# Kernel optimization log

Hardware: AMD Instinct MI355X
Metric: run time of the kernel (lower is better)

Reference implementation:

```python
import jax, jax.numpy as jnp
import numpy as np

N_RELS = 8           # NUM_BASE_RELS(6) + 2
CONF_LOG_WEIGHT = 0.1
LN_EPS = 1e-5


def setup_inputs() -> dict:
    key = jax.random.key(0)
    ks = jax.random.split(key, 10)
    N, E, IN, H, R, L = 100000, 1600000, 128, 64, 16, 2
    x = jax.random.normal(ks[0], (N, IN), jnp.float32)
    edge_index = jax.random.randint(ks[1], (2, E), 0, N, jnp.int32)
    edge_type = jax.random.randint(ks[2], (E,), 0, N_RELS, jnp.int32)
    edge_attr = jax.random.uniform(ks[3], (E, 1), jnp.float32)

    def init(k, shape, fan_in):
        return jax.random.normal(k, shape, jnp.float32) * (1.0 / np.sqrt(fan_in))

    W_in = init(ks[4], (IN, H), IN)
    b_in = jnp.zeros((H,), jnp.float32)
    W_msg = init(ks[5], (L, H, H), H)          # msg_lin, no bias
    rel_emb = init(ks[6], (L, N_RELS, R), 1.0)  # relation embedding tables
    W_relproj = init(ks[7], (L, R, H), R)       # rel_proj, no bias
    att_vec = init(ks[8], (L, 3 * H), 3 * H)
    bias = jnp.zeros((L, H), jnp.float32)
    ln_g = jnp.ones((L, H), jnp.float32)
    ln_b = jnp.zeros((L, H), jnp.float32)
    return dict(x=x, W_in=W_in, b_in=b_in, W_msg=W_msg, rel_emb=rel_emb,
                W_relproj=W_relproj, att_vec=att_vec, bias=bias,
                ln_g=ln_g, ln_b=ln_b, edge_attr=edge_attr,
                edge_index=edge_index, edge_type=edge_type)


def _layer(h, src, dst, t, conf, W_msg, rel_emb, W_relproj, att_vec, bias, N, H):
    h_src = h[src] @ W_msg                      # [E,H] gather + linear
    h_dst = h[dst] @ W_msg                      # [E,H]
    r = rel_emb[t] @ W_relproj                  # [E,H]
    a_dst, a_src, a_rel = att_vec[:H], att_vec[H:2 * H], att_vec[2 * H:]
    # equivalent to sum over concat([h_dst, h_src, r]) * att_vec
    e = h_dst @ a_dst + h_src @ a_src + r @ a_rel      # [E]
    e = jax.nn.leaky_relu(e, 0.2)
    e = e + CONF_LOG_WEIGHT * jnp.log(jnp.maximum(conf, 1e-6))
    # segment softmax over destination nodes
    m = jax.ops.segment_max(e, dst, num_segments=N)
    ex = jnp.exp(e - m[dst])
    s = jax.ops.segment_sum(ex, dst, num_segments=N)
    alpha = ex / s[dst]
    out = jax.ops.segment_sum(h_src * alpha[:, None], dst, num_segments=N)
    return out + bias


def _layernorm(x, g, b):
    mu = x.mean(-1, keepdims=True)
    var = ((x - mu) ** 2).mean(-1, keepdims=True)
    return (x - mu) / jnp.sqrt(var + LN_EPS) * g + b


def reference(x, W_in, b_in, W_msg, rel_emb, W_relproj, att_vec, bias, ln_g, ln_b,
              edge_attr, edge_index, edge_type):
    N, H = x.shape[0], W_in.shape[1]
    src, dst = edge_index[0], edge_index[1]
    t = jnp.clip(edge_type, 0, N_RELS - 1)
    conf = edge_attr[:, 0]
    h = jax.nn.relu(x @ W_in + b_in)            # in_lin + relu (dropout eval = id)
    for l in range(W_msg.shape[0]):
        out = _layer(h, src, dst, t, conf, W_msg[l], rel_emb[l], W_relproj[l],
                     att_vec[l], bias[l], N, H)
        h = _layernorm(h + jax.nn.relu(out), ln_g[l], ln_b[l])
    return h
```

## Files before the change

kernel.cpp:

```cpp
#include <hip/hip_runtime.h>
#include <math.h>

#define H 64
#define IN_DIM 128
#define NRELS 8
#define SCAN_B 512
#define DEGCAP 128
#define CHUNK 8192
#define MAXBUCK 512
#define BUCKSZ 2048

__global__ __launch_bounds__(256) void k_input(const float* __restrict__ x,
    const float* __restrict__ W_in, const float* __restrict__ b_in,
    float* __restrict__ h, int N) {
  __shared__ __align__(16) float Ws[IN_DIM * H];
  __shared__ __align__(16) float xs[16 * IN_DIM];
  const float4* W4 = (const float4*)W_in;
  float4* Ws4 = (float4*)Ws;
  for (int i = threadIdx.x; i < IN_DIM * H / 4; i += 256) Ws4[i] = W4[i];
  int base = blockIdx.x * 16;
  const float4* x4 = (const float4*)x;
  float4* xs4 = (float4*)xs;
  for (int i = threadIdx.x; i < 16 * IN_DIM / 4; i += 256) {
    int nn = base + (i >> 5);
    xs4[i] = (nn < N) ? x4[(size_t)nn * 32 + (i & 31)]
                      : make_float4(0.f, 0.f, 0.f, 0.f);
  }
  __syncthreads();
  int wid = threadIdx.x >> 6, lane = threadIdx.x & 63;
  int n0 = base + wid * 4;
  float a0 = 0.f, a1 = 0.f, a2 = 0.f, a3 = 0.f;
  const float4* xr4 = (const float4*)(xs + wid * 4 * IN_DIM);
  #pragma unroll 4
  for (int kq = 0; kq < IN_DIM / 4; ++kq) {
    float4 f0 = xr4[kq];
    float4 f1 = xr4[32 + kq];
    float4 f2 = xr4[64 + kq];
    float4 f3 = xr4[96 + kq];
    int k = kq * 4;
    float w0 = Ws[(k + 0) * H + lane];
    float w1 = Ws[(k + 1) * H + lane];
    float w2 = Ws[(k + 2) * H + lane];
    float w3 = Ws[(k + 3) * H + lane];
    a0 = fmaf(f0.x, w0, a0); a0 = fmaf(f0.y, w1, a0);
    a0 = fmaf(f0.z, w2, a0); a0 = fmaf(f0.w, w3, a0);
    a1 = fmaf(f1.x, w0, a1); a1 = fmaf(f1.y, w1, a1);
    a1 = fmaf(f1.z, w2, a1); a1 = fmaf(f1.w, w3, a1);
    a2 = fmaf(f2.x, w0, a2); a2 = fmaf(f2.y, w1, a2);
    a2 = fmaf(f2.z, w2, a2); a2 = fmaf(f2.w, w3, a2);
    a3 = fmaf(f3.x, w0, a3); a3 = fmaf(f3.y, w1, a3);
    a3 = fmaf(f3.z, w2, a3); a3 = fmaf(f3.w, w3, a3);
  }
  float bb = b_in[lane];
  if (n0 + 0 < N) h[(size_t)(n0 + 0) * H + lane] = fmaxf(a0 + bb, 0.f);
  if (n0 + 1 < N) h[(size_t)(n0 + 1) * H + lane] = fmaxf(a1 + bb, 0.f);
  if (n0 + 2 < N) h[(size_t)(n0 + 2) * H + lane] = fmaxf(a2 + bb, 0.f);
  if (n0 + 3 < N) h[(size_t)(n0 + 3) * H + lane] = fmaxf(a3 + bb, 0.f);
}

__global__ __launch_bounds__(SCAN_B) void k_scan1(const int* __restrict__ deg,
    int* __restrict__ inc, int* __restrict__ bsum, int N) {
  __shared__ int sm[SCAN_B];
  int g = blockIdx.x * SCAN_B + threadIdx.x;
  sm[threadIdx.x] = (g < N) ? deg[g] : 0;
  __syncthreads();
  for (int o = 1; o < SCAN_B; o <<= 1) {
    int t = (threadIdx.x >= o) ? sm[threadIdx.x - o] : 0;
    __syncthreads();
    sm[threadIdx.x] += t;
    __syncthreads();
  }
  if (g < N) inc[g] = sm[threadIdx.x];
  if (threadIdx.x == SCAN_B - 1) bsum[blockIdx.x] = sm[threadIdx.x];
}

__global__ __launch_bounds__(SCAN_B) void k_scan2(int* __restrict__ bsum, int nb) {
  __shared__ int sm[SCAN_B];
  __shared__ int carry;
  if (threadIdx.x == 0) carry = 0;
  __syncthreads();
  for (int base = 0; base < nb; base += SCAN_B) {
    int i = base + threadIdx.x;
    sm[threadIdx.x] = (i < nb) ? bsum[i] : 0;
    __syncthreads();
    if (threadIdx.x == 0) {
      int run = carry;
      int lim = nb - base < SCAN_B ? nb - base : SCAN_B;
      for (int j = 0; j < lim; ++j) { run += sm[j]; sm[j] = run; }
      carry = run;
    }
    __syncthreads();
    if (i < nb) bsum[i] = sm[threadIdx.x];
    __syncthreads();
  }
}

__global__ __launch_bounds__(SCAN_B) void k_scan3(const int* __restrict__ inc,
    const int* __restrict__ bsum, const int* __restrict__ deg,
    int* __restrict__ row, int N) {
  int g = blockIdx.x * SCAN_B + threadIdx.x;
  if (g >= N) return;
  int off = (blockIdx.x > 0) ? bsum[blockIdx.x - 1] : 0;
  int end = inc[g] + off;
  row[g] = end - deg[g];
  if (g == N - 1) row[N] = end;
}

__global__ __launch_bounds__(SCAN_B) void k_scan3b(const int* __restrict__ inc,
    const int* __restrict__ bsum, const int* __restrict__ cnt,
    int* __restrict__ woff, int M) {
  int g = blockIdx.x * SCAN_B + threadIdx.x;
  if (g >= M) return;
  int off = (blockIdx.x > 0) ? bsum[blockIdx.x - 1] : 0;
  woff[g] = inc[g] + off - cnt[g];
}

__global__ __launch_bounds__(256) void k_bhist(const int* __restrict__ ei,
    int* __restrict__ counts, int E, int nwg, int nbuck, int bshift) {
  __shared__ int cnt[MAXBUCK];
  for (int b = threadIdx.x; b < nbuck; b += 256) cnt[b] = 0;
  __syncthreads();
  int wg = blockIdx.x;
  int lo = wg * CHUNK, hi = lo + CHUNK < E ? lo + CHUNK : E;
  for (int j = lo + threadIdx.x; j < hi; j += 256)
    atomicAdd(&cnt[ei[E + j] >> bshift], 1);
  __syncthreads();
  for (int b = threadIdx.x; b < nbuck; b += 256)
    counts[(size_t)b * nwg + wg] = cnt[b];
}

__global__ __launch_bounds__(256) void k_binscat(const int* __restrict__ ei,
    const int* __restrict__ et, const float* __restrict__ ea,
    const int* __restrict__ woff, int4* __restrict__ staged,
    int E, int nwg, int nbuck, int bshift) {
  __shared__ int cur[MAXBUCK];
  int wg = blockIdx.x;
  for (int b = threadIdx.x; b < nbuck; b += 256)
    cur[b] = woff[(size_t)b * nwg + wg];
  __syncthreads();
  int lo = wg * CHUNK, hi = lo + CHUNK < E ? lo + CHUNK : E;
  for (int j = lo + threadIdx.x; j < hi; j += 256) {
    int s = ei[j], d = ei[E + j];
    int t = et[j]; t = t < 0 ? 0 : (t > NRELS - 1 ? NRELS - 1 : t);
    float cl = 0.1f * logf(fmaxf(ea[j], 1e-6f));
    int pos = atomicAdd(&cur[d >> bshift], 1);
    staged[pos] = make_int4(s | (t << 20), d, __float_as_int(cl), 0);
  }
}

__global__ __launch_bounds__(256) void k_hist2(const int* __restrict__ staged,
    const int* __restrict__ woff, int* __restrict__ deg,
    int E, int nwg, int nbuck, int bshift, int N) {
  __shared__ int cnt[BUCKSZ];
  int b = blockIdx.x;
  int nbase = b << bshift;
  int nn = N - nbase; if (nn > (1 << bshift)) nn = 1 << bshift;
  for (int i = threadIdx.x; i < nn; i += 256) cnt[i] = 0;
  __syncthreads();
  int lo = woff[(size_t)b * nwg];
  int hi = (b + 1 < nbuck) ? woff[(size_t)(b + 1) * nwg] : E;
  for (int j = lo + threadIdx.x; j < hi; j += 256)
    atomicAdd(&cnt[staged[j * 4 + 1] - nbase], 1);
  __syncthreads();
  for (int i = threadIdx.x; i < nn; i += 256) deg[nbase + i] = cnt[i];
}

__global__ __launch_bounds__(256) void k_scat2(const int4* __restrict__ staged,
    const int* __restrict__ woff, const int* __restrict__ row,
    int2* __restrict__ erec, int E, int nwg, int nbuck, int bshift, int N) {
  __shared__ int cur[BUCKSZ];
  int b = blockIdx.x;
  int nbase = b << bshift;
  int nn = N - nbase; if (nn > (1 << bshift)) nn = 1 << bshift;
  for (int i = threadIdx.x; i < nn; i += 256) cur[i] = row[nbase + i];
  __syncthreads();
  int lo = woff[(size_t)b * nwg];
  int hi = (b + 1 < nbuck) ? woff[(size_t)(b + 1) * nwg] : E;
  for (int j = lo + threadIdx.x; j < hi; j += 256) {
    int4 r = staged[j];
    int pos = atomicAdd(&cur[r.y - nbase], 1);
    erec[pos] = make_int2(r.x, r.z);
  }
}

__global__ __launch_bounds__(256) void k_node(const float* __restrict__ h,
    const float* __restrict__ Wmsg, const float* __restrict__ att,
    float* __restrict__ hw, float* __restrict__ esrc, float* __restrict__ edst,
    int N) {
  __shared__ __align__(16) float Ws[H * H];
  __shared__ __align__(16) float hs[16 * H];
  const float4* W4 = (const float4*)Wmsg;
  float4* Ws4 = (float4*)Ws;
  for (int i = threadIdx.x; i < H * H / 4; i += 256) Ws4[i] = W4[i];
  int base = blockIdx.x * 16;
  const float4* h4 = (const float4*)h;
  float4* hs4 = (float4*)hs;
  for (int i = threadIdx.x; i < 16 * H / 4; i += 256) {
    int nn = base + (i >> 4);
    hs4[i] = (nn < N) ? h4[(size_t)nn * 16 + (i & 15)]
                      : make_float4(0.f, 0.f, 0.f, 0.f);
  }
  __syncthreads();
  int wid = threadIdx.x >> 6, lane = threadIdx.x & 63;
  int n0 = base + wid * 4;
  float a0 = 0.f, a1 = 0.f, a2 = 0.f, a3 = 0.f;
  const float4* hr4 = (const float4*)(hs + wid * 4 * H);
  #pragma unroll 4
  for (int kq = 0; kq < H / 4; ++kq) {
    float4 f0 = hr4[kq];
    float4 f1 = hr4[16 + kq];
    float4 f2 = hr4[32 + kq];
    float4 f3 = hr4[48 + kq];
    int k = kq * 4;
    float w0 = Ws[(k + 0) * H + lane];
    float w1 = Ws[(k + 1) * H + lane];
    float w2 = Ws[(k + 2) * H + lane];
    float w3 = Ws[(k + 3) * H + lane];
    a0 = fmaf(f0.x, w0, a0); a0 = fmaf(f0.y, w1, a0);
    a0 = fmaf(f0.z, w2, a0); a0 = fmaf(f0.w, w3, a0);
    a1 = fmaf(f1.x, w0, a1); a1 = fmaf(f1.y, w1, a1);
    a1 = fmaf(f1.z, w2, a1); a1 = fmaf(f1.w, w3, a1);
    a2 = fmaf(f2.x, w0, a2); a2 = fmaf(f2.y, w1, a2);
    a2 = fmaf(f2.z, w2, a2); a2 = fmaf(f2.w, w3, a2);
    a3 = fmaf(f3.x, w0, a3); a3 = fmaf(f3.y, w1, a3);
    a3 = fmaf(f3.z, w2, a3); a3 = fmaf(f3.w, w3, a3);
  }
  float ad = att[lane], as = att[H + lane];
  float acc[4] = {a0, a1, a2, a3};
  #pragma unroll
  for (int i = 0; i < 4; ++i) {
    int n = n0 + i;
    if (n >= N) break;
    hw[(size_t)n * H + lane] = acc[i];
    float vd = acc[i] * ad, vs = acc[i] * as;
    #pragma unroll
    for (int o = 32; o >= 1; o >>= 1) {
      vd += __shfl_xor(vd, o);
      vs += __shfl_xor(vs, o);
    }
    if (lane == 0) { edst[n] = vd; esrc[n] = vs; }
  }
}

__global__ void k_rel(const float* __restrict__ rel_emb,
    const float* __restrict__ Wrp, const float* __restrict__ att,
    float* __restrict__ erel, int R) {
  int l = blockIdx.x;
  int r = threadIdx.x >> 6, lane = threadIdx.x & 63;
  const float* re = rel_emb + ((size_t)l * NRELS + r) * R;
  const float* wp = Wrp + (size_t)l * R * H;
  float acc = 0.f;
  for (int k = 0; k < R; ++k) acc = fmaf(re[k], wp[k * H + lane], acc);
  float v = acc * att[(size_t)l * 3 * H + 2 * H + lane];
  #pragma unroll
  for (int o = 32; o >= 1; o >>= 1) v += __shfl_xor(v, o);
  if (lane == 0) erel[l * NRELS + r] = v;
}

__global__ __launch_bounds__(256) void k_agg(const int* __restrict__ row,
    const int2* __restrict__ erec, const float* __restrict__ esrc,
    const float* __restrict__ edst, const float* __restrict__ erel,
    const float* __restrict__ hw, const float* __restrict__ h,
    const float* __restrict__ bias, const float* __restrict__ ln_g,
    const float* __restrict__ ln_b, float* __restrict__ hout, int N) {
  __shared__ float er[NRELS];
  __shared__ float els[4][DEGCAP];
  __shared__ int   sls[4][DEGCAP];
  if (threadIdx.x < NRELS) er[threadIdx.x] = erel[threadIdx.x];
  __syncthreads();
  int wid = threadIdx.x >> 6, lane = threadIdx.x & 63;
  int w = blockIdx.x * 4 + wid;
  if (w >= N) return;
  int st = row[w], en = row[w + 1];
  int deg = en - st;
  float ed = edst[w];
  float m = -3.4e38f;
  float acc = 0.f, ssum = 0.f;

  if (deg <= DEGCAP) {
    for (int j = st + lane; j < en; j += 64) {
      int2 r = erec[j];
      int sj = r.x & 0xFFFFF;
      float e = ed + esrc[sj] + er[(r.x >> 20) & 7];
      e = e > 0.f ? e : 0.2f * e;
      e += __int_as_float(r.y);
      els[wid][j - st] = e;
      sls[wid][j - st] = sj;
      m = fmaxf(m, e);
    }
    #pragma unroll
    for (int o = 32; o >= 1; o >>= 1) m = fmaxf(m, __shfl_xor(m, o));
    int k = 0;
    for (; k + 8 <= deg; k += 8) {
      int s0 = sls[wid][k],     s1 = sls[wid][k + 1];
      int s2 = sls[wid][k + 2], s3 = sls[wid][k + 3];
      int s4 = sls[wid][k + 4], s5 = sls[wid][k + 5];
      int s6 = sls[wid][k + 6], s7 = sls[wid][k + 7];
      float h0 = hw[(size_t)s0 * H + lane];
      float h1 = hw[(size_t)s1 * H + lane];
      float h2 = hw[(size_t)s2 * H + lane];
      float h3 = hw[(size_t)s3 * H + lane];
      float h4 = hw[(size_t)s4 * H + lane];
      float h5 = hw[(size_t)s5 * H + lane];
      float h6 = hw[(size_t)s6 * H + lane];
      float h7 = hw[(size_t)s7 * H + lane];
      float p0 = __expf(els[wid][k] - m);
      float p1 = __expf(els[wid][k + 1] - m);
      float p2 = __expf(els[wid][k + 2] - m);
      float p3 = __expf(els[wid][k + 3] - m);
      float p4 = __expf(els[wid][k + 4] - m);
      float p5 = __expf(els[wid][k + 5] - m);
      float p6 = __expf(els[wid][k + 6] - m);
      float p7 = __expf(els[wid][k + 7] - m);
      ssum += p0; acc = fmaf(h0, p0, acc);
      ssum += p1; acc = fmaf(h1, p1, acc);
      ssum += p2; acc = fmaf(h2, p2, acc);
      ssum += p3; acc = fmaf(h3, p3, acc);
      ssum += p4; acc = fmaf(h4, p4, acc);
      ssum += p5; acc = fmaf(h5, p5, acc);
      ssum += p6; acc = fmaf(h6, p6, acc);
      ssum += p7; acc = fmaf(h7, p7, acc);
    }
    for (; k + 4 <= deg; k += 4) {
      int s0 = sls[wid][k],     s1 = sls[wid][k + 1];
      int s2 = sls[wid][k + 2], s3 = sls[wid][k + 3];
      float h0 = hw[(size_t)s0 * H + lane];
      float h1 = hw[(size_t)s1 * H + lane];
      float h2 = hw[(size_t)s2 * H + lane];
      float h3 = hw[(size_t)s3 * H + lane];
      float p0 = __expf(els[wid][k] - m);
      float p1 = __expf(els[wid][k + 1] - m);
      float p2 = __expf(els[wid][k + 2] - m);
      float p3 = __expf(els[wid][k + 3] - m);
      ssum += p0; acc = fmaf(h0, p0, acc);
      ssum += p1; acc = fmaf(h1, p1, acc);
      ssum += p2; acc = fmaf(h2, p2, acc);
      ssum += p3; acc = fmaf(h3, p3, acc);
    }
    for (; k < deg; ++k) {
      int sj = sls[wid][k];
      float hv = hw[(size_t)sj * H + lane];
      float p = __expf(els[wid][k] - m);
      ssum += p; acc = fmaf(hv, p, acc);
    }
  } else {
    for (int j = st + lane; j < en; j += 64) {
      int2 r = erec[j];
      float e = ed + esrc[r.x & 0xFFFFF] + er[(r.x >> 20) & 7];
      e = e > 0.f ? e : 0.2f * e;
      m = fmaxf(m, e + __int_as_float(r.y));
    }
    #pragma unroll
    for (int o = 32; o >= 1; o >>= 1) m = fmaxf(m, __shfl_xor(m, o));
    for (int j = st; j < en; ++j) {
      int2 r = erec[j];
      int sj = r.x & 0xFFFFF;
      float e = ed + esrc[sj] + er[(r.x >> 20) & 7];
      e = e > 0.f ? e : 0.2f * e;
      e += __int_as_float(r.y);
      float p = __expf(e - m);
      ssum += p;
      acc = fmaf(hw[(size_t)sj * H + lane], p, acc);
    }
  }

  float o = (deg > 0) ? acc / ssum : 0.f;
  o += bias[lane];
  float v = h[(size_t)w * H + lane] + fmaxf(o, 0.f);
  float mu = v;
  #pragma unroll
  for (int off = 32; off >= 1; off >>= 1) mu += __shfl_xor(mu, off);
  mu *= (1.f / 64.f);
  float dv = v - mu;
  float var = dv * dv;
  #pragma unroll
  for (int off = 32; off >= 1; off >>= 1) var += __shfl_xor(var, off);
  var *= (1.f / 64.f);
  hout[(size_t)w * H + lane] = dv * rsqrtf(var + 1e-5f) * ln_g[lane] + ln_b[lane];
}

extern "C" void kernel_launch(void* const* d_in, const int* in_sizes, int n_in,
                              void* d_out, int out_size, void* d_ws, size_t ws_size,
                              hipStream_t stream) {
  const float* x       = (const float*)d_in[0];
  const float* W_in    = (const float*)d_in[1];
  const float* b_in    = (const float*)d_in[2];
  const float* W_msg   = (const float*)d_in[3];
  const float* rel_emb = (const float*)d_in[4];
  const float* W_rp    = (const float*)d_in[5];
  const float* att     = (const float*)d_in[6];
  const float* bias    = (const float*)d_in[7];
  const float* ln_g    = (const float*)d_in[8];
  const float* ln_b    = (const float*)d_in[9];
  const float* ea      = (const float*)d_in[10];
  const int*   ei      = (const int*)d_in[11];
  const int*   et      = (const int*)d_in[12];

  int N = in_sizes[0] / IN_DIM;
  int E = in_sizes[12];
  int L = in_sizes[7] / H;
  int R = in_sizes[5] / (L * H);
  int nb = (N + SCAN_B - 1) / SCAN_B;

  int bshift = 9;
  while (((N + (1 << bshift) - 1) >> bshift) > MAXBUCK) bshift++;
  int nbuck = (N + (1 << bshift) - 1) >> bshift;
  int nwg = (E + CHUNK - 1) / CHUNK;
  int M = nbuck * nwg;
  int nb2 = (M + SCAN_B - 1) / SCAN_B;

  float* ws   = (float*)d_ws;
  float* h    = ws;
  float* hw   = h + (size_t)N * H;
  int4* staged = (int4*)hw;
  size_t hwElems = (size_t)N * H;
  size_t stagedElems = ((size_t)E * 4 + 3) & ~(size_t)3;
  size_t region2 = hwElems > stagedElems ? hwElems : stagedElems;
  int2*  erec = (int2*)(hw + region2);
  float* esrc = (float*)(erec + E);
  float* edst = esrc + N;
  float* erel = edst + N;
  int* row    = (int*)(erel + L * NRELS);
  int* deg    = row + N + 1;
  int* inc    = deg + N;
  int* bsum   = inc + N;
  int* counts = bsum + nb;
  int* cinc   = counts + M;
  int* woff   = cinc + M;
  int* bsum2  = woff + M;

  int nb16 = (N + 15) / 16;
  k_input<<<nb16, 256, 0, stream>>>(x, W_in, b_in, h, N);

  k_bhist<<<nwg, 256, 0, stream>>>(ei, counts, E, nwg, nbuck, bshift);
  k_scan1<<<nb2, SCAN_B, 0, stream>>>(counts, cinc, bsum2, M);
  k_scan2<<<1, SCAN_B, 0, stream>>>(bsum2, nb2);
  k_scan3b<<<nb2, SCAN_B, 0, stream>>>(cinc, bsum2, counts, woff, M);
  k_binscat<<<nwg, 256, 0, stream>>>(ei, et, ea, woff, staged, E, nwg, nbuck, bshift);

  k_hist2<<<nbuck, 256, 0, stream>>>((const int*)staged, woff, deg, E, nwg, nbuck, bshift, N);
  k_scan1<<<nb, SCAN_B, 0, stream>>>(deg, inc, bsum, N);
  k_scan2<<<1, SCAN_B, 0, stream>>>(bsum, nb);
  k_scan3<<<nb, SCAN_B, 0, stream>>>(inc, bsum, deg, row, N);
  k_scat2<<<nbuck, 256, 0, stream>>>(staged, woff, row, erec, E, nwg, nbuck, bshift, N);

  k_rel<<<L, 512, 0, stream>>>(rel_emb, W_rp, att, erel, R);

  for (int l = 0; l < L; ++l) {
    k_node<<<nb16, 256, 0, stream>>>(h, W_msg + (size_t)l * H * H,
                                     att + (size_t)l * 3 * H, hw, esrc, edst, N);
    float* hout = (l == L - 1) ? (float*)d_out : h;
    k_agg<<<(N + 3) / 4, 256, 0, stream>>>(row, erec, esrc, edst,
                                           erel + (size_t)l * NRELS, hw, h,
                                           bias + (size_t)l * H,
                                           ln_g + (size_t)l * H,
                                           ln_b + (size_t)l * H, hout, N);
  }
}
```

Baseline: 488.5 us.

## Aggregate raw features then apply W_msg per node, folding attention vectors

Uses linearity to move the message linear layer after the softmax aggregation: the attention logits are computed from precomputed W_msg·att vectors, and each node multiplies its aggregated raw h by W_msg inside k_agg. This removes the separate k_node pass and the hw buffer write/read, and fuses the next layer's per-node logit projections into the previous kernel's epilogue, with ping-pong buffers. In exchange k_agg loads W_msg into shared memory per block, processes 4 nodes per wave serially, and changes floating-point summation order.

```diff
diff --git a/kernel.cpp b/kernel.cpp
--- a/kernel.cpp
+++ b/kernel.cpp
@@ -10,9 +10,22 @@
 #define MAXBUCK 512
 #define BUCKSZ 2048
 
+__global__ void k_wvec(const float* __restrict__ Wmsg, const float* __restrict__ att,
+                       float* __restrict__ wdst, float* __restrict__ wsrc) {
+  int l = blockIdx.x, k = threadIdx.x;
+  const float* W  = Wmsg + ((size_t)l * H + k) * H;
+  const float* ad = att + (size_t)l * 3 * H;
+  const float* as = ad + H;
+  float sd = 0.f, ss = 0.f;
+  for (int j = 0; j < H; ++j) { float w = W[j]; sd = fmaf(w, ad[j], sd); ss = fmaf(w, as[j], ss); }
+  wdst[l * H + k] = sd;
+  wsrc[l * H + k] = ss;
+}
+
 __global__ __launch_bounds__(256) void k_input(const float* __restrict__ x,
     const float* __restrict__ W_in, const float* __restrict__ b_in,
-    float* __restrict__ h, int N) {
+    const float* __restrict__ wsrc0, const float* __restrict__ wdst0,
+    float* __restrict__ h, float* __restrict__ esrc, float* __restrict__ edst, int N) {
   __shared__ __align__(16) float Ws[IN_DIM * H];
   __shared__ __align__(16) float xs[16 * IN_DIM];
   const float4* W4 = (const float4*)W_in;
@@ -52,10 +65,22 @@
     a3 = fmaf(f3.z, w2, a3); a3 = fmaf(f3.w, w3, a3);
   }
   float bb = b_in[lane];
-  if (n0 + 0 < N) h[(size_t)(n0 + 0) * H + lane] = fmaxf(a0 + bb, 0.f);
-  if (n0 + 1 < N) h[(size_t)(n0 + 1) * H + lane] = fmaxf(a1 + bb, 0.f);
-  if (n0 + 2 < N) h[(size_t)(n0 + 2) * H + lane] = fmaxf(a2 + bb, 0.f);
-  if (n0 + 3 < N) h[(size_t)(n0 + 3) * H + lane] = fmaxf(a3 + bb, 0.f);
+  float wsn = wsrc0[lane], wdn = wdst0[lane];
+  float vals[4] = {fmaxf(a0 + bb, 0.f), fmaxf(a1 + bb, 0.f),
+                   fmaxf(a2 + bb, 0.f), fmaxf(a3 + bb, 0.f)};
+  #pragma unroll
+  for (int i = 0; i < 4; ++i) {
+    int n = n0 + i;
+    if (n >= N) break;
+    h[(size_t)n * H + lane] = vals[i];
+    float vs = vals[i] * wsn, vd = vals[i] * wdn;
+    #pragma unroll
+    for (int o = 32; o >= 1; o >>= 1) {
+      vs += __shfl_xor(vs, o);
+      vd += __shfl_xor(vd, o);
+    }
+    if (lane == 0) { esrc[n] = vs; edst[n] = vd; }
+  }
 }
 
 __global__ __launch_bounds__(SCAN_B) void k_scan1(const int* __restrict__ deg,
@@ -183,65 +208,6 @@
   }
 }
 
-__global__ __launch_bounds__(256) void k_node(const float* __restrict__ h,
-    const float* __restrict__ Wmsg, const float* __restrict__ att,
-    float* __restrict__ hw, float* __restrict__ esrc, float* __restrict__ edst,
-    int N) {
-  __shared__ __align__(16) float Ws[H * H];
-  __shared__ __align__(16) float hs[16 * H];
-  const float4* W4 = (const float4*)Wmsg;
-  float4* Ws4 = (float4*)Ws;
-  for (int i = threadIdx.x; i < H * H / 4; i += 256) Ws4[i] = W4[i];
-  int base = blockIdx.x * 16;
-  const float4* h4 = (const float4*)h;
-  float4* hs4 = (float4*)hs;
-  for (int i = threadIdx.x; i < 16 * H / 4; i += 256) {
-    int nn = base + (i >> 4);
-    hs4[i] = (nn < N) ? h4[(size_t)nn * 16 + (i & 15)]
-                      : make_float4(0.f, 0.f, 0.f, 0.f);
-  }
-  __syncthreads();
-  int wid = threadIdx.x >> 6, lane = threadIdx.x & 63;
-  int n0 = base + wid * 4;
-  float a0 = 0.f, a1 = 0.f, a2 = 0.f, a3 = 0.f;
-  const float4* hr4 = (const float4*)(hs + wid * 4 * H);
-  #pragma unroll 4
-  for (int kq = 0; kq < H / 4; ++kq) {
-    float4 f0 = hr4[kq];
-    float4 f1 = hr4[16 + kq];
-    float4 f2 = hr4[32 + kq];
-    float4 f3 = hr4[48 + kq];
-    int k = kq * 4;
-    float w0 = Ws[(k + 0) * H + lane];
-    float w1 = Ws[(k + 1) * H + lane];
-    float w2 = Ws[(k + 2) * H + lane];
-    float w3 = Ws[(k + 3) * H + lane];
-    a0 = fmaf(f0.x, w0, a0); a0 = fmaf(f0.y, w1, a0);
-    a0 = fmaf(f0.z, w2, a0); a0 = fmaf(f0.w, w3, a0);
-    a1 = fmaf(f1.x, w0, a1); a1 = fmaf(f1.y, w1, a1);
-    a1 = fmaf(f1.z, w2, a1); a1 = fmaf(f1.w, w3, a1);
-    a2 = fmaf(f2.x, w0, a2); a2 = fmaf(f2.y, w1, a2);
-    a2 = fmaf(f2.z, w2, a2); a2 = fmaf(f2.w, w3, a2);
-    a3 = fmaf(f3.x, w0, a3); a3 = fmaf(f3.y, w1, a3);
-    a3 = fmaf(f3.z, w2, a3); a3 = fmaf(f3.w, w3, a3);
-  }
-  float ad = att[lane], as = att[H + lane];
-  float acc[4] = {a0, a1, a2, a3};
-  #pragma unroll
-  for (int i = 0; i < 4; ++i) {
-    int n = n0 + i;
-    if (n >= N) break;
-    hw[(size_t)n * H + lane] = acc[i];
-    float vd = acc[i] * ad, vs = acc[i] * as;
-    #pragma unroll
-    for (int o = 32; o >= 1; o >>= 1) {
-      vd += __shfl_xor(vd, o);
-      vs += __shfl_xor(vs, o);
-    }
-    if (lane == 0) { edst[n] = vd; esrc[n] = vs; }
-  }
-}
-
 __global__ void k_rel(const float* __restrict__ rel_emb,
     const float* __restrict__ Wrp, const float* __restrict__ att,
     float* __restrict__ erel, int R) {
@@ -260,123 +226,158 @@
 __global__ __launch_bounds__(256) void k_agg(const int* __restrict__ row,
     const int2* __restrict__ erec, const float* __restrict__ esrc,
     const float* __restrict__ edst, const float* __restrict__ erel,
-    const float* __restrict__ hw, const float* __restrict__ h,
+    const float* __restrict__ Wmsg, const float* __restrict__ hin,
     const float* __restrict__ bias, const float* __restrict__ ln_g,
-    const float* __restrict__ ln_b, float* __restrict__ hout, int N) {
+    const float* __restrict__ ln_b,
+    const float* __restrict__ wsrc_n, const float* __restrict__ wdst_n,
+    float* __restrict__ esrc_o, float* __restrict__ edst_o,
+    float* __restrict__ hout, int N, int last) {
   __shared__ float er[NRELS];
+  __shared__ __align__(16) float Ws[H * H];
+  __shared__ __align__(16) float aggs[4][H];
   __shared__ float els[4][DEGCAP];
   __shared__ int   sls[4][DEGCAP];
+  const float4* W4 = (const float4*)Wmsg;
+  float4* Ws4 = (float4*)Ws;
+  for (int i = threadIdx.x; i < H * H / 4; i += 256) Ws4[i] = W4[i];
   if (threadIdx.x < NRELS) er[threadIdx.x] = erel[threadIdx.x];
   __syncthreads();
   int wid = threadIdx.x >> 6, lane = threadIdx.x & 63;
-  int w = blockIdx.x * 4 + wid;
-  if (w >= N) return;
-  int st = row[w], en = row[w + 1];
-  int deg = en - st;
-  float ed = edst[w];
-  float m = -3.4e38f;
-  float acc = 0.f, ssum = 0.f;
-
-  if (deg <= DEGCAP) {
-    for (int j = st + lane; j < en; j += 64) {
-      int2 r = erec[j];
-      int sj = r.x & 0xFFFFF;
-      float e = ed + esrc[sj] + er[(r.x >> 20) & 7];
-      e = e > 0.f ? e : 0.2f * e;
-      e += __int_as_float(r.y);
-      els[wid][j - st] = e;
-      sls[wid][j - st] = sj;
-      m = fmaxf(m, e);
+  float bb = bias[lane], lg = ln_g[lane], lb = ln_b[lane];
+  float wsn = last ? 0.f : wsrc_n[lane];
+  float wdn = last ? 0.f : wdst_n[lane];
+  int base = blockIdx.x * 16 + wid * 4;
+
+  for (int ii = 0; ii < 4; ++ii) {
+    int w = base + ii;
+    if (w >= N) break;
+    int st = row[w], en = row[w + 1];
+    int deg = en - st;
+    float ed = edst[w];
+    float m = -3.4e38f, agg = 0.f, ssum = 0.f;
+
+    if (deg <= DEGCAP) {
+      for (int j = st + lane; j < en; j += 64) {
+        int2 r = erec[j];
+        int sj = r.x & 0xFFFFF;
+        float e = ed + esrc[sj] + er[(r.x >> 20) & 7];
+        e = e > 0.f ? e : 0.2f * e;
+        e += __int_as_float(r.y);
+        els[wid][j - st] = e;
+        sls[wid][j - st] = sj;
+        m = fmaxf(m, e);
+      }
+      #pragma unroll
+      for (int o = 32; o >= 1; o >>= 1) m = fmaxf(m, __shfl_xor(m, o));
+      int k = 0;
+      for (; k + 8 <= deg; k += 8) {
+        int s0 = sls[wid][k],     s1 = sls[wid][k + 1];
+        int s2 = sls[wid][k + 2], s3 = sls[wid][k + 3];
+        int s4 = sls[wid][k + 4], s5 = sls[wid][k + 5];
+        int s6 = sls[wid][k + 6], s7 = sls[wid][k + 7];
+        float h0 = hin[(size_t)s0 * H + lane];
+        float h1 = hin[(size_t)s1 * H + lane];
+        float h2 = hin[(size_t)s2 * H + lane];
+        float h3 = hin[(size_t)s3 * H + lane];
+        float h4 = hin[(size_t)s4 * H + lane];
+        float h5 = hin[(size_t)s5 * H + lane];
+        float h6 = hin[(size_t)s6 * H + lane];
+        float h7 = hin[(size_t)s7 * H + lane];
+        float p0 = __expf(els[wid][k] - m);
+        float p1 = __expf(els[wid][k + 1] - m);
+        float p2 = __expf(els[wid][k + 2] - m);
+        float p3 = __expf(els[wid][k + 3] - m);
+        float p4 = __expf(els[wid][k + 4] - m);
+        float p5 = __expf(els[wid][k + 5] - m);
+        float p6 = __expf(els[wid][k + 6] - m);
+        float p7 = __expf(els[wid][k + 7] - m);
+        ssum += p0; agg = fmaf(h0, p0, agg);
+        ssum += p1; agg = fmaf(h1, p1, agg);
+        ssum += p2; agg = fmaf(h2, p2, agg);
+        ssum += p3; agg = fmaf(h3, p3, agg);
+        ssum += p4; agg = fmaf(h4, p4, agg);
+        ssum += p5; agg = fmaf(h5, p5, agg);
+        ssum += p6; agg = fmaf(h6, p6, agg);
+        ssum += p7; agg = fmaf(h7, p7, agg);
+      }
+      for (; k + 4 <= deg; k += 4) {
+        int s0 = sls[wid][k],     s1 = sls[wid][k + 1];
+        int s2 = sls[wid][k + 2], s3 = sls[wid][k + 3];
+        float h0 = hin[(size_t)s0 * H + lane];
+        float h1 = hin[(size_t)s1 * H + lane];
+        float h2 = hin[(size_t)s2 * H + lane];
+        float h3 = hin[(size_t)s3 * H + lane];
+        float p0 = __expf(els[wid][k] - m);
+        float p1 = __expf(els[wid][k + 1] - m);
+        float p2 = __expf(els[wid][k + 2] - m);
+        float p3 = __expf(els[wid][k + 3] - m);
+        ssum += p0; agg = fmaf(h0, p0, agg);
+        ssum += p1; agg = fmaf(h1, p1, agg);
+        ssum += p2; agg = fmaf(h2, p2, agg);
+        ssum += p3; agg = fmaf(h3, p3, agg);
+      }
+      for (; k < deg; ++k) {
+        int sj = sls[wid][k];
+        float hv = hin[(size_t)sj * H + lane];
+        float p = __expf(els[wid][k] - m);
+        ssum += p; agg = fmaf(hv, p, agg);
+      }
+    } else {
+      for (int j = st + lane; j < en; j += 64) {
+        int2 r = erec[j];
+        float e = ed + esrc[r.x & 0xFFFFF] + er[(r.x >> 20) & 7];
+        e = e > 0.f ? e : 0.2f * e;
+        m = fmaxf(m, e + __int_as_float(r.y));
+      }
+      #pragma unroll
+      for (int o = 32; o >= 1; o >>= 1) m = fmaxf(m, __shfl_xor(m, o));
+      for (int j = st; j < en; ++j) {
+        int2 r = erec[j];
+        int sj = r.x & 0xFFFFF;
+        float e = ed + esrc[sj] + er[(r.x >> 20) & 7];
+        e = e > 0.f ? e : 0.2f * e;
+        e += __int_as_float(r.y);
+        float p = __expf(e - m);
+        ssum += p;
+        agg = fmaf(hin[(size_t)sj * H + lane], p, agg);
+      }
     }
+
+    aggs[wid][lane] = (deg > 0) ? agg / ssum : 0.f;
+    float out = 0.f;
+    const float4* ag4 = (const float4*)aggs[wid];
     #pragma unroll
-    for (int o = 32; o >= 1; o >>= 1) m = fmaxf(m, __shfl_xor(m, o));
-    int k = 0;
-    for (; k + 8 <= deg; k += 8) {
-      int s0 = sls[wid][k],     s1 = sls[wid][k + 1];
-      int s2 = sls[wid][k + 2], s3 = sls[wid][k + 3];
-      int s4 = sls[wid][k + 4], s5 = sls[wid][k + 5];
-      int s6 = sls[wid][k + 6], s7 = sls[wid][k + 7];
-      float h0 = hw[(size_t)s0 * H + lane];
-      float h1 = hw[(size_t)s1 * H + lane];
-      float h2 = hw[(size_t)s2 * H + lane];
-      float h3 = hw[(size_t)s3 * H + lane];
-      float h4 = hw[(size_t)s4 * H + lane];
-      float h5 = hw[(size_t)s5 * H + lane];
-      float h6 = hw[(size_t)s6 * H + lane];
-      float h7 = hw[(size_t)s7 * H + lane];
-      float p0 = __expf(els[wid][k] - m);
-      float p1 = __expf(els[wid][k + 1] - m);
-      float p2 = __expf(els[wid][k + 2] - m);
-      float p3 = __expf(els[wid][k + 3] - m);
-      float p4 = __expf(els[wid][k + 4] - m);
-      float p5 = __expf(els[wid][k + 5] - m);
-      float p6 = __expf(els[wid][k + 6] - m);
-      float p7 = __expf(els[wid][k + 7] - m);
-      ssum += p0; acc = fmaf(h0, p0, acc);
-      ssum += p1; acc = fmaf(h1, p1, acc);
-      ssum += p2; acc = fmaf(h2, p2, acc);
-      ssum += p3; acc = fmaf(h3, p3, acc);
-      ssum += p4; acc = fmaf(h4, p4, acc);
-      ssum += p5; acc = fmaf(h5, p5, acc);
-      ssum += p6; acc = fmaf(h6, p6, acc);
-      ssum += p7; acc = fmaf(h7, p7, acc);
+    for (int kq = 0; kq < H / 4; ++kq) {
+      float4 a = ag4[kq];
+      int k = kq * 4;
+      out = fmaf(a.x, Ws[(k + 0) * H + lane], out);
+      out = fmaf(a.y, Ws[(k + 1) * H + lane], out);
+      out = fmaf(a.z, Ws[(k + 2) * H + lane], out);
+      out = fmaf(a.w, Ws[(k + 3) * H + lane], out);
     }
-    for (; k + 4 <= deg; k += 4) {
-      int s0 = sls[wid][k],     s1 = sls[wid][k + 1];
-      int s2 = sls[wid][k + 2], s3 = sls[wid][k + 3];
-      float h0 = hw[(size_t)s0 * H + lane];
-      float h1 = hw[(size_t)s1 * H + lane];
-      float h2 = hw[(size_t)s2 * H + lane];
-      float h3 = hw[(size_t)s3 * H + lane];
-      float p0 = __expf(els[wid][k] - m);
-      float p1 = __expf(els[wid][k + 1] - m);
-      float p2 = __expf(els[wid][k + 2] - m);
-      float p3 = __expf(els[wid][k + 3] - m);
-      ssum += p0; acc = fmaf(h0, p0, acc);
-      ssum += p1; acc = fmaf(h1, p1, acc);
-      ssum += p2; acc = fmaf(h2, p2, acc);
-      ssum += p3; acc = fmaf(h3, p3, acc);
+    out += bb;
+    float v = hin[(size_t)w * H + lane] + fmaxf(out, 0.f);
+    float mu = v;
+    #pragma unroll
+    for (int off = 32; off >= 1; off >>= 1) mu += __shfl_xor(mu, off);
+    mu *= (1.f / 64.f);
+    float dv = v - mu;
+    float var = dv * dv;
+    #pragma unroll
+    for (int off = 32; off >= 1; off >>= 1) var += __shfl_xor(var, off);
+    var *= (1.f / 64.f);
+    float res = dv * rsqrtf(var + 1e-5f) * lg + lb;
+    hout[(size_t)w * H + lane] = res;
+    if (!last) {
+      float vs = res * wsn, vd = res * wdn;
+      #pragma unroll
+      for (int o = 32; o >= 1; o >>= 1) {
+        vs += __shfl_xor(vs, o);
+        vd += __shfl_xor(vd, o);
+      }
+      if (lane == 0) { esrc_o[w] = vs; edst_o[w] = vd; }
     }
-    for (; k < deg; ++k) {
-      int sj = sls[wid][k];
-      float hv = hw[(size_t)sj * H + lane];
-      float p = __expf(els[wid][k] - m);
-      ssum += p; acc = fmaf(hv, p, acc);
-    }
-  } else {
-    for (int j = st + lane; j < en; j += 64) {
-      int2 r = erec[j];
-      float e = ed + esrc[r.x & 0xFFFFF] + er[(r.x >> 20) & 7];
-      e = e > 0.f ? e : 0.2f * e;
-      m = fmaxf(m, e + __int_as_float(r.y));
-    }
-    #pragma unroll
-    for (int o = 32; o >= 1; o >>= 1) m = fmaxf(m, __shfl_xor(m, o));
-    for (int j = st; j < en; ++j) {
-      int2 r = erec[j];
-      int sj = r.x & 0xFFFFF;
-      float e = ed + esrc[sj] + er[(r.x >> 20) & 7];
-      e = e > 0.f ? e : 0.2f * e;
-      e += __int_as_float(r.y);
-      float p = __expf(e - m);
-      ssum += p;
-      acc = fmaf(hw[(size_t)sj * H + lane], p, acc);
-    }
-  }
-
-  float o = (deg > 0) ? acc / ssum : 0.f;
-  o += bias[lane];
-  float v = h[(size_t)w * H + lane] + fmaxf(o, 0.f);
-  float mu = v;
-  #pragma unroll
-  for (int off = 32; off >= 1; off >>= 1) mu += __shfl_xor(mu, off);
-  mu *= (1.f / 64.f);
-  float dv = v - mu;
-  float var = dv * dv;
-  #pragma unroll
-  for (int off = 32; off >= 1; off >>= 1) var += __shfl_xor(var, off);
-  var *= (1.f / 64.f);
-  hout[(size_t)w * H + lane] = dv * rsqrtf(var + 1e-5f) * ln_g[lane] + ln_b[lane];
+  }
 }
 
 extern "C" void kernel_launch(void* const* d_in, const int* in_sizes, int n_in,
@@ -410,17 +411,21 @@
   int nb2 = (M + SCAN_B - 1) / SCAN_B;
 
   float* ws   = (float*)d_ws;
-  float* h    = ws;
-  float* hw   = h + (size_t)N * H;
-  int4* staged = (int4*)hw;
-  size_t hwElems = (size_t)N * H;
+  float* h0   = ws;
+  float* h1   = h0 + (size_t)N * H;
+  int4* staged = (int4*)h1;
+  size_t hElems = (size_t)N * H;
   size_t stagedElems = ((size_t)E * 4 + 3) & ~(size_t)3;
-  size_t region2 = hwElems > stagedElems ? hwElems : stagedElems;
-  int2*  erec = (int2*)(hw + region2);
-  float* esrc = (float*)(erec + E);
-  float* edst = esrc + N;
-  float* erel = edst + N;
-  int* row    = (int*)(erel + L * NRELS);
+  size_t region2 = hElems > stagedElems ? hElems : stagedElems;
+  int2*  erec  = (int2*)(h1 + region2);
+  float* esrcA = (float*)(erec + E);
+  float* edstA = esrcA + N;
+  float* esrcB = edstA + N;
+  float* edstB = esrcB + N;
+  float* erel  = edstB + N;
+  float* wdst  = erel + (size_t)L * NRELS;
+  float* wsrc  = wdst + (size_t)L * H;
+  int* row    = (int*)(wsrc + (size_t)L * H);
   int* deg    = row + N + 1;
   int* inc    = deg + N;
   int* bsum   = inc + N;
@@ -429,8 +434,10 @@
   int* woff   = cinc + M;
   int* bsum2  = woff + M;
 
+  k_wvec<<<L, H, 0, stream>>>(W_msg, att, wdst, wsrc);
+
   int nb16 = (N + 15) / 16;
-  k_input<<<nb16, 256, 0, stream>>>(x, W_in, b_in, h, N);
+  k_input<<<nb16, 256, 0, stream>>>(x, W_in, b_in, wsrc, wdst, h0, esrcA, edstA, N);
 
   k_bhist<<<nwg, 256, 0, stream>>>(ei, counts, E, nwg, nbuck, bshift);
   k_scan1<<<nb2, SCAN_B, 0, stream>>>(counts, cinc, bsum2, M);
@@ -447,13 +454,21 @@
   k_rel<<<L, 512, 0, stream>>>(rel_emb, W_rp, att, erel, R);
 
   for (int l = 0; l < L; ++l) {
-    k_node<<<nb16, 256, 0, stream>>>(h, W_msg + (size_t)l * H * H,
-                                     att + (size_t)l * 3 * H, hw, esrc, edst, N);
-    float* hout = (l == L - 1) ? (float*)d_out : h;
-    k_agg<<<(N + 3) / 4, 256, 0, stream>>>(row, erec, esrc, edst,
-                                           erel + (size_t)l * NRELS, hw, h,
-                                           bias + (size_t)l * H,
-                                           ln_g + (size_t)l * H,
-                                           ln_b + (size_t)l * H, hout, N);
-  }
-}
+    int last = (l == L - 1);
+    const float* hin  = (l & 1) ? h1 : h0;
+    float* hout = last ? (float*)d_out : ((l & 1) ? h0 : h1);
+    const float* esI = (l & 1) ? esrcB : esrcA;
+    const float* edI = (l & 1) ? edstB : edstA;
+    float* esO = (l & 1) ? esrcA : esrcB;
+    float* edO = (l & 1) ? edstA : edstB;
+    k_agg<<<nb16, 256, 0, stream>>>(row, erec, esI, edI,
+                                    erel + (size_t)l * NRELS,
+                                    W_msg + (size_t)l * H * H, hin,
+                                    bias + (size_t)l * H,
+                                    ln_g + (size_t)l * H,
+                                    ln_b + (size_t)l * H,
+                                    last ? wsrc : wsrc + (size_t)(l + 1) * H,
+                                    last ? wdst : wdst + (size_t)(l + 1) * H,
+                                    esO, edO, hout, N, last);
+  }
+}
```

After: 451.8 us. -7.5%, faster.
